# Kernel optimization log

Measured on AMD Instinct MI355X. Metric: run time of the kernel, lower is better.

## Reference

```python
import jax, jax.numpy as jnp
import numpy as np

N_NODES = 20000
N_EDGES = 320000
N_GRAPHS = 32
IN_CH = 5
HID = 64
HEADS = 4
DH = HID // HEADS  # 16
LAYERS = 8
EPS = 1e-5
SLOPE = 0.2


def setup_inputs() -> dict:
    key = jax.random.key(0)
    ks = jax.random.split(key, 32)
    inp = {}
    inp['x1'] = jax.random.normal(ks[0], (N_NODES, IN_CH), dtype=jnp.float32)
    inp['x2'] = jax.random.normal(ks[1], (N_NODES, IN_CH), dtype=jnp.float32)
    inp['edge_index1'] = jax.random.randint(ks[2], (2, N_EDGES), 0, N_NODES, dtype=jnp.int32)
    inp['edge_index2'] = jax.random.randint(ks[3], (2, N_EDGES), 0, N_NODES, dtype=jnp.int32)
    inp['batch1'] = jnp.sort(jax.random.randint(ks[4], (N_NODES,), 0, N_GRAPHS, dtype=jnp.int32))
    inp['batch2'] = jnp.sort(jax.random.randint(ks[5], (N_NODES,), 0, N_GRAPHS, dtype=jnp.int32))
    # node_lin
    inp['Wn'] = jax.random.normal(ks[6], (IN_CH, HID), dtype=jnp.float32) / np.sqrt(IN_CH)
    inp['bnode'] = jnp.zeros((HID,), dtype=jnp.float32)
    # GATv2 layers (stacked over LAYERS)
    s = 1.0 / np.sqrt(HID)
    inp['Wl'] = jax.random.normal(ks[7], (LAYERS, HID, HID), dtype=jnp.float32) * s
    inp['bl'] = jnp.zeros((LAYERS, HID), dtype=jnp.float32)
    inp['Wr'] = jax.random.normal(ks[8], (LAYERS, HID, HID), dtype=jnp.float32) * s
    inp['br'] = jnp.zeros((LAYERS, HID), dtype=jnp.float32)
    inp['att'] = jax.random.normal(ks[9], (LAYERS, HEADS, DH), dtype=jnp.float32) / np.sqrt(DH)
    inp['cbias'] = jnp.zeros((LAYERS, HID), dtype=jnp.float32)
    # batch norms
    inp['gamma'] = jnp.ones((LAYERS, HID), dtype=jnp.float32)
    inp['beta'] = jnp.zeros((LAYERS, HID), dtype=jnp.float32)
    # fc head
    inp['f1w'] = jax.random.normal(ks[10], (2 * HID, 256), dtype=jnp.float32) / np.sqrt(2 * HID)
    inp['f1b'] = jnp.zeros((256,), dtype=jnp.float32)
    inp['f2w'] = jax.random.normal(ks[11], (256, 128), dtype=jnp.float32) / np.sqrt(256)
    inp['f2b'] = jnp.zeros((128,), dtype=jnp.float32)
    inp['f3w'] = jax.random.normal(ks[12], (128, 1), dtype=jnp.float32) / np.sqrt(128)
    inp['f3b'] = jnp.zeros((1,), dtype=jnp.float32)
    return inp


def _gatv2_layer(x, src, dst, Wl, bl, Wr, br, att, bias):
    # x: [N, HID]; src/dst: [E'] (self loops included)
    N = x.shape[0]
    xl = (x @ Wl + bl).reshape(N, HEADS, DH)  # source transform
    xr = (x @ Wr + br).reshape(N, HEADS, DH)  # target transform
    e = jax.nn.leaky_relu(xl[src] + xr[dst], SLOPE)          # [E, H, DH]
    score = jnp.einsum('ehd,hd->eh', e, att)                  # [E, H]
    smax = jax.ops.segment_max(score, dst, num_segments=N)    # [N, H]
    ex = jnp.exp(score - smax[dst])
    denom = jax.ops.segment_sum(ex, dst, num_segments=N)
    alpha = ex / denom[dst]                                   # [E, H]
    msg = alpha[:, :, None] * xl[src]                         # [E, H, DH]
    out = jax.ops.segment_sum(msg, dst, num_segments=N)       # [N, H, DH]
    return out.reshape(N, HID) + bias


def _forward_once(x, edge_index, batch, Wn, bnode, Wl, bl, Wr, br, att, cbias, gamma, beta):
    N = x.shape[0]
    loop = jnp.arange(N, dtype=edge_index.dtype)
    src = jnp.concatenate([edge_index[0], loop])  # add_self_loops=True
    dst = jnp.concatenate([edge_index[1], loop])
    h = x @ Wn + bnode
    for l in range(LAYERS):
        g = _gatv2_layer(h, src, dst, Wl[l], bl[l], Wr[l], br[l], att[l], cbias[l])
        mu = g.mean(axis=0)
        var = g.var(axis=0)
        g = (g - mu) / jnp.sqrt(var + EPS) * gamma[l] + beta[l]
        h = h + jax.nn.elu(g)
    # global_mean_pool
    sums = jax.ops.segment_sum(h, batch, num_segments=N_GRAPHS)
    cnt = jax.ops.segment_sum(jnp.ones((N,), dtype=h.dtype), batch, num_segments=N_GRAPHS)
    return sums / jnp.maximum(cnt, 1.0)[:, None]


def reference(x1, edge_index1, batch1, x2, edge_index2, batch2, Wn, bnode, Wl, bl, Wr, br, att, cbias, gamma, beta, f1w, f1b, f2w, f2b, f3w, f3b):
    o1 = _forward_once(x1, edge_index1, batch1, Wn, bnode, Wl, bl, Wr, br, att, cbias, gamma, beta)
    o2 = _forward_once(x2, edge_index2, batch2, Wn, bnode, Wl, bl, Wr, br, att, cbias, gamma, beta)
    c = jnp.concatenate([o1, o2], axis=1)           # [G, 128]
    h = jax.nn.relu(c @ f1w + f1b)                   # dropout = identity (eval)
    h = jax.nn.relu(h @ f2w + f2b)
    return h @ f3w + f3b                             # [G, 1]
```

## Files before the change

kernel.cpp:

```cpp
#include <hip/hip_runtime.h>
#include <hip/hip_bf16.h>
#include <hip/hip_fp16.h>
#include <stdint.h>

#define N_NODES 20000
#define HID 64
#define EPS 1e-5f

typedef _Float16 h2 __attribute__((ext_vector_type(2)));

__device__ __forceinline__ h2 u2h(uint32_t u) { union { uint32_t u; h2 h; } v; v.u = u; return v.h; }

struct GP {
    const int* ei;
    const int* batch;
    const float* x;
    int* deg;
    int* cursor;
    int* csr;
    float* h;
    __half* xlh;
    __half* xrh;
    float* gb;
    float* stats;
    float* osum;
};


__global__ void k_csr_init(GP a, GP b, int n, int two) {
    int t = blockIdx.x * blockDim.x + threadIdx.x;
    if (t < n) {
        a.deg[t] = 1;
        if (two) b.deg[t] = 1;
    }
}

__global__ void k_count(GP a, GP b, int Ea, int Eb, int two) {
    int t = blockIdx.x * blockDim.x + threadIdx.x;
    if (t < Ea) atomicAdd(&a.deg[a.ei[Ea + t]], 1);
    if (two && t < Eb) atomicAdd(&b.deg[b.ei[Eb + t]], 1);
}

#define SCAN_T 1024
#define SCAN_C 20
__global__ __launch_bounds__(1024) void k_scan(GP a, GP b, int n, int totA, int totB) {
    GP g = blockIdx.x ? b : a;
    int total = blockIdx.x ? totB : totA;
    __shared__ int sd[SCAN_T];
    int t = threadIdx.x;
    int base = t * SCAN_C;
    int loc[SCAN_C];
    int s = 0;
#pragma unroll
    for (int i = 0; i < SCAN_C; ++i) {
        int idx = base + i;
        loc[i] = (idx < n) ? g.deg[idx] : 0;
        s += loc[i];
    }
    sd[t] = s;
    __syncthreads();
    for (int off = 1; off < SCAN_T; off <<= 1) {
        int v = (t >= off) ? sd[t - off] : 0;
        __syncthreads();
        sd[t] += v;
        __syncthreads();
    }
    int run = sd[t] - s;
#pragma unroll
    for (int i = 0; i < SCAN_C; ++i) {
        int idx = base + i;
        if (idx < n) { g.deg[idx] = run; g.cursor[idx] = run; run += loc[i]; }
    }
    if (t == 0) g.deg[n] = total;
}

__global__ void k_scatter(GP a, GP b, int Ea, int Eb, int n, int two) {
    int t = blockIdx.x * blockDim.x + threadIdx.x;
    if (t < Ea) {
        int s = a.ei[t], d = a.ei[Ea + t];
        a.csr[atomicAdd(&a.cursor[d], 1)] = s * 128;
    } else if (t < Ea + n) {
        int nn = t - Ea;
        a.csr[atomicAdd(&a.cursor[nn], 1)] = nn * 128;
    }
    if (two) {
        if (t < Eb) {
            int s = b.ei[t], d = b.ei[Eb + t];
            b.csr[atomicAdd(&b.cursor[d], 1)] = s * 128;
        } else if (t < Eb + n) {
            int nn = t - Eb;
            b.csr[atomicAdd(&b.cursor[nn], 1)] = nn * 128;
        }
    }
}


__global__ void k_wcvt(const float* __restrict__ Wl, const float* __restrict__ Wr,
                       uint32_t* __restrict__ wpk) {
    int t = blockIdx.x * 256 + threadIdx.x;
    if (t >= 16384) return;
    int l = t >> 11, r = t & 2047;
    int k2 = r >> 6, c = r & 63;
    const float* wl = Wl + l * 4096;
    const float* wr = Wr + l * 4096;
    h2 a, b;
    a.x = (_Float16)wl[(2 * k2) * 64 + c];
    a.y = (_Float16)wl[(2 * k2 + 1) * 64 + c];
    b.x = (_Float16)wr[(2 * k2) * 64 + c];
    b.y = (_Float16)wr[(2 * k2 + 1) * 64 + c];
    union { h2 h; uint32_t u; } ua, ub;
    ua.h = a; ub.h = b;
    wpk[l * 4096 + r] = ua.u;
    wpk[l * 4096 + 2048 + r] = ub.u;
}


__global__ void k_nodelin(GP a, GP b, int nPer, const float* __restrict__ Wn,
                          const float* __restrict__ bn, int n) {
    int bid = blockIdx.x;
    GP g = a;
    if (bid >= nPer) { g = b; bid -= nPer; }
    int idx = bid * 256 + threadIdx.x;
    if (idx >= n * HID) return;
    int node = idx >> 6, c = idx & 63;
    float acc = bn[c];
#pragma unroll
    for (int k = 0; k < 5; ++k) acc += g.x[node * 5 + k] * Wn[k * HID + c];
    g.h[idx] = acc;
}


__global__ __launch_bounds__(256) void k_lin2(GP ga, GP gbp, int nPer, int n,
        const uint32_t* __restrict__ wl2g, const float* __restrict__ bl,
        const uint32_t* __restrict__ wr2g, const float* __restrict__ br,
        const float* __restrict__ gamma, const float* __restrict__ beta, int layer) {
    __shared__ uint32_t wl2[2048], wr2[2048];
    __shared__ _Float16 hs16[2048];
    int bid = blockIdx.x;
    GP g = ga;
    if (bid >= nPer) { g = gbp; bid -= nPer; }
    {
        uint4* dl = (uint4*)wl2; const uint4* sl = (const uint4*)wl2g;
        uint4* dr = (uint4*)wr2; const uint4* sr = (const uint4*)wr2g;
        for (int i = threadIdx.x; i < 512; i += 256) { dl[i] = sl[i]; dr[i] = sr[i]; }
    }
    int c = threadIdx.x & 63;
    int wid = threadIdx.x >> 6;
    float blv = bl[c], brv = br[c];
    float mu = 0.f, inv = 1.f, gam = 1.f, bet = 0.f;
    if (layer > 0) {
        const float* st = g.stats + (layer - 1) * 128;
        float invn = 1.0f / (float)n;
        mu = st[c] * invn;
        float var = st[64 + c] * invn - mu * mu;
        inv = rsqrtf(fmaxf(var, 0.f) + EPS);
        gam = gamma[c]; bet = beta[c];
    }
    int nb = bid * 32 + wid * 8;
    size_t off0 = (size_t)nb * 64 + c;
    float hv[8];
    if (layer > 0) {
#pragma unroll
        for (int j = 0; j < 8; ++j) {
            float gv = g.gb[off0 + j * 64];
            float ov = g.h[off0 + j * 64];
            float v = (gv - mu) * inv * gam + bet;
            v = v > 0.f ? v : expm1f(v);
            hv[j] = ov + v;
            g.h[off0 + j * 64] = hv[j];
        }
    } else {
#pragma unroll
        for (int j = 0; j < 8; ++j) hv[j] = g.h[off0 + j * 64];
    }
    _Float16* hw16 = &hs16[wid * 512];
#pragma unroll
    for (int j = 0; j < 8; ++j) hw16[j * 64 + c] = (_Float16)hv[j];
    __syncthreads();
    const uint32_t* hw2 = (const uint32_t*)hw16;
    float accl[8], accr[8];
#pragma unroll
    for (int j = 0; j < 8; ++j) { accl[j] = blv; accr[j] = brv; }
    for (int k8 = 0; k8 < 8; ++k8) {
        uint4 hq[8];
#pragma unroll
        for (int j = 0; j < 8; ++j) hq[j] = *(const uint4*)&hw2[j * 32 + k8 * 4];
#pragma unroll
        for (int p = 0; p < 4; ++p) {
            h2 wlv = u2h(wl2[(k8 * 4 + p) * 64 + c]);
            h2 wrv = u2h(wr2[(k8 * 4 + p) * 64 + c]);
#pragma unroll
            for (int j = 0; j < 8; ++j) {
                h2 hp = u2h((&hq[j].x)[p]);
                accl[j] = __builtin_amdgcn_fdot2(hp, wlv, accl[j], false);
                accr[j] = __builtin_amdgcn_fdot2(hp, wrv, accr[j], false);
            }
        }
    }
#pragma unroll
    for (int j = 0; j < 8; ++j) {
        g.xlh[off0 + j * 64] = __float2half(accl[j]);
        g.xrh[off0 + j * 64] = __float2half(accr[j]);
    }
}


__device__ __forceinline__ float red8(float p) {
    p += __int_as_float(__builtin_amdgcn_update_dpp(0, __float_as_int(p), 0xB1, 0xF, 0xF, true));
    p += __int_as_float(__builtin_amdgcn_update_dpp(0, __float_as_int(p), 0x4E, 0xF, 0xF, true));
    p += __int_as_float(__builtin_amdgcn_update_dpp(0, __float_as_int(p), 0x141, 0xF, 0xF, true));
    return p;
}

__global__ __launch_bounds__(1024) void k_attn(GP ga, GP gbp, int nPer,
        const float* __restrict__ att, const float* __restrict__ cbias, int layer, int n) {
    int bid = blockIdx.x;
    GP g = (bid & 1) ? gbp : ga;
    bid >>= 1;
    int lane = threadIdx.x & 63;
    int wid = threadIdx.x >> 6;
    int hh = lane >> 5;
    int cl = lane & 31;
    int gw = bid * 16 + wid;
    int nw = nPer * 16;
    const float LOG2E = 1.44269504f;
    float a0 = att[2 * cl] * LOG2E;
    float a1 = att[2 * cl + 1] * LOG2E;
    float cb0 = cbias[2 * cl], cb1 = cbias[2 * cl + 1];
    const h2 slope = {(_Float16)0.2f, (_Float16)0.2f};
    const int* __restrict__ rowptr = g.deg;
    const int* __restrict__ csr = g.csr;
    const char* xlb = (const char*)g.xlh + (size_t)cl * 4;
    const char* xrb = (const char*)g.xrh + (size_t)cl * 4;
    float* __restrict__ gbuf = g.gb;
    float* st = g.stats + layer * 128;
    float bs0 = 0.f, bs1 = 0.f, bq0 = 0.f, bq1 = 0.f;
    for (int node = gw; node < n; node += nw) {
        int start = rowptr[node], end = rowptr[node + 1];
        h2 xrv = *(const h2*)(xrb + (size_t)node * 128);
        float sself;
        {
            h2 xs = *(const h2*)(xlb + (size_t)node * 128);
            h2 t = xs + xrv;
            h2 lk = __builtin_elementwise_max(t, t * slope);
            float sp = fmaf((float)lk.x, a0, (float)lk.y * a1);
            sself = red8(sp);
        }
        float lsum = 0.f, acc0 = 0.f, acc1 = 0.f;
        int idx = start;
        for (; idx + 16 <= end; idx += 16) {
            int off[8];
            h2 xv[8];
#pragma unroll
            for (int j = 0; j < 8; ++j) off[j] = csr[idx + 2 * j + hh];
#pragma unroll
            for (int j = 0; j < 8; ++j) xv[j] = *(const h2*)(xlb + off[j]);
#pragma unroll
            for (int j = 0; j < 8; ++j) {
                h2 t = xv[j] + xrv;
                h2 lk = __builtin_elementwise_max(t, t * slope);
                float sp = fmaf((float)lk.x, a0, (float)lk.y * a1);
                float w = exp2f(fminf(red8(sp) - sself, 110.f));
                lsum += w;
                acc0 = fmaf(w, (float)xv[j].x, acc0);
                acc1 = fmaf(w, (float)xv[j].y, acc1);
            }
        }
        for (; idx + 8 <= end; idx += 8) {
            int off[4];
            h2 xv[4];
#pragma unroll
            for (int j = 0; j < 4; ++j) off[j] = csr[idx + 2 * j + hh];
#pragma unroll
            for (int j = 0; j < 4; ++j) xv[j] = *(const h2*)(xlb + off[j]);
#pragma unroll
            for (int j = 0; j < 4; ++j) {
                h2 t = xv[j] + xrv;
                h2 lk = __builtin_elementwise_max(t, t * slope);
                float sp = fmaf((float)lk.x, a0, (float)lk.y * a1);
                float w = exp2f(fminf(red8(sp) - sself, 110.f));
                lsum += w;
                acc0 = fmaf(w, (float)xv[j].x, acc0);
                acc1 = fmaf(w, (float)xv[j].y, acc1);
            }
        }
        for (; idx < end; idx += 2) {
            int e = idx + hh;
            bool valid = e < end;
            int off = csr[valid ? e : end - 1];
            h2 xv = *(const h2*)(xlb + off);
            h2 t = xv + xrv;
            h2 lk = __builtin_elementwise_max(t, t * slope);
            float sp = fmaf((float)lk.x, a0, (float)lk.y * a1);
            float w = exp2f(fminf(red8(sp) - sself, 110.f));
            w = valid ? w : 0.f;
            lsum += w;
            acc0 = fmaf(w, (float)xv.x, acc0);
            acc1 = fmaf(w, (float)xv.y, acc1);
        }
        lsum += __shfl_xor(lsum, 32);
        acc0 += __shfl_xor(acc0, 32);
        acc1 += __shfl_xor(acc1, 32);
        if (hh == 0) {
            float invl = 1.0f / lsum;
            float o0 = acc0 * invl + cb0;
            float o1 = acc1 * invl + cb1;
            float2 o = {o0, o1};
            *(float2*)(gbuf + (size_t)node * 64 + 2 * cl) = o;
            bs0 += o0; bs1 += o1;
            bq0 += o0 * o0; bq1 += o1 * o1;
        }
    }
    __shared__ float2 sred[1024];
    float2 z = {0.f, 0.f};
    float2 v1 = {bs0, bs1};
    sred[threadIdx.x] = (hh == 0) ? v1 : z;
    __syncthreads();
    if (threadIdx.x < 32) {
        float t0 = 0.f, t1 = 0.f;
#pragma unroll
        for (int w = 0; w < 16; ++w) { float2 s = sred[w * 64 + threadIdx.x]; t0 += s.x; t1 += s.y; }
        atomicAdd(&st[2 * threadIdx.x], t0);
        atomicAdd(&st[2 * threadIdx.x + 1], t1);
    }
    __syncthreads();
    float2 v2 = {bq0, bq1};
    sred[threadIdx.x] = (hh == 0) ? v2 : z;
    __syncthreads();
    if (threadIdx.x < 32) {
        float t0 = 0.f, t1 = 0.f;
#pragma unroll
        for (int w = 0; w < 16; ++w) { float2 s = sred[w * 64 + threadIdx.x]; t0 += s.x; t1 += s.y; }
        atomicAdd(&st[64 + 2 * threadIdx.x], t0);
        atomicAdd(&st[64 + 2 * threadIdx.x + 1], t1);
    }
}


__global__ __launch_bounds__(256) void k_pool(GP ga, GP gbp, int nPer,
        const float* __restrict__ gamma, const float* __restrict__ beta, int n) {
    int bid = blockIdx.x;
    GP g = ga;
    if (bid >= nPer) { g = gbp; bid -= nPer; }
    int lane = threadIdx.x & 63, w = threadIdx.x >> 6;
    const float* st = g.stats + 7 * 128;
    float invn = 1.f / (float)n;
    float mu = st[lane] * invn;
    float var = st[64 + lane] * invn - mu * mu;
    float inv = rsqrtf(fmaxf(var, 0.f) + EPS);
    float gam = gamma[lane], bet = beta[lane];
    int chunk = (n + nPer - 1) / nPer;
    int s = bid * chunk;
    int e = min(s + chunk, n);
    float acc = 0.f;
    int cur = -1;
    for (int node = s + w; node < e; node += 4) {
        int bg = g.batch[node];
        size_t off = (size_t)node * 64 + lane;
        float gv = g.gb[off];
        float hv = g.h[off];
        float v = (gv - mu) * inv * gam + bet;
        float hn = hv + (v > 0.f ? v : expm1f(v));
        if (bg != cur) {
            if (cur >= 0) atomicAdd(&g.osum[cur * 64 + lane], acc);
            acc = 0.f; cur = bg;
        }
        acc += hn;
    }
    if (cur >= 0) atomicAdd(&g.osum[cur * 64 + lane], acc);
}


__device__ __forceinline__ int lb(const int* __restrict__ b, int n, int v) {
    int lo = 0, hi = n;
    while (lo < hi) { int mid = (lo + hi) >> 1; if (b[mid] < v) lo = mid + 1; else hi = mid; }
    return lo;
}

__global__ __launch_bounds__(256) void k_fc(const float* __restrict__ o1, const float* __restrict__ o2,
                                            const int* __restrict__ b1, const int* __restrict__ b2,
                                            const float* __restrict__ f1w, const float* __restrict__ f1b,
                                            const float* __restrict__ f2w, const float* __restrict__ f2b,
                                            const float* __restrict__ f3w, const float* __restrict__ f3b,
                                            float* __restrict__ out, int n) {
    int gid = blockIdx.x, t = threadIdx.x;
    __shared__ float cin[128];
    __shared__ float h1[256];
    __shared__ float red[128];
    __shared__ int cnts[2];
    if (t == 0) cnts[0] = lb(b1, n, gid + 1) - lb(b1, n, gid);
    if (t == 1) cnts[1] = lb(b2, n, gid + 1) - lb(b2, n, gid);
    __syncthreads();
    if (t < 64) {
        float c1 = (float)(cnts[0] > 0 ? cnts[0] : 1);
        float c2 = (float)(cnts[1] > 0 ? cnts[1] : 1);
        cin[t] = o1[gid * 64 + t] / c1;
        cin[64 + t] = o2[gid * 64 + t] / c2;
    }
    __syncthreads();
    float a = f1b[t];
#pragma unroll 8
    for (int k = 0; k < 128; ++k) a += cin[k] * f1w[k * 256 + t];
    h1[t] = fmaxf(a, 0.f);
    __syncthreads();
    if (t < 128) {
        float a2 = f2b[t];
#pragma unroll 8
        for (int k = 0; k < 256; ++k) a2 += h1[k] * f2w[k * 128 + t];
        red[t] = fmaxf(a2, 0.f) * f3w[t];
    }
    __syncthreads();
    for (int off = 64; off > 0; off >>= 1) {
        if (t < off) red[t] += red[t + off];
        __syncthreads();
    }
    if (t == 0) out[gid] = red[0] + f3b[0];
}


extern "C" void kernel_launch(void* const* d_in, const int* in_sizes, int n_in,
                              void* d_out, int out_size, void* d_ws, size_t ws_size,
                              hipStream_t stream) {
    const float* x1 = (const float*)d_in[0];
    const float* x2 = (const float*)d_in[1];
    const int* ei1 = (const int*)d_in[2];
    const int* ei2 = (const int*)d_in[3];
    const int* b1 = (const int*)d_in[4];
    const int* b2 = (const int*)d_in[5];
    const float* Wn = (const float*)d_in[6];
    const float* bnode = (const float*)d_in[7];
    const float* Wl = (const float*)d_in[8];
    const float* bl = (const float*)d_in[9];
    const float* Wr = (const float*)d_in[10];
    const float* br = (const float*)d_in[11];
    const float* att = (const float*)d_in[12];
    const float* cbias = (const float*)d_in[13];
    const float* gamma = (const float*)d_in[14];
    const float* beta = (const float*)d_in[15];
    const float* f1w = (const float*)d_in[16];
    const float* f1b = (const float*)d_in[17];
    const float* f2w = (const float*)d_in[18];
    const float* f2b = (const float*)d_in[19];
    const float* f3w = (const float*)d_in[20];
    const float* f3b = (const float*)d_in[21];
    float* out = (float*)d_out;

    const int N = N_NODES;
    const int EA = in_sizes[2] / 2;
    const int EB = in_sizes[3] / 2;
    const size_t INT_PG = 20096 + 20096 + 340096;
    const size_t BIG = (size_t)N * 64;
    const size_t SMALL = 2 * 1024 + 2 * 2048;
    const size_t WPK = 32768;
    const size_t dualBytes = 2 * INT_PG * 4 + (8 * BIG + SMALL + WPK) * 4;
    const int dual = (ws_size >= dualBytes) ? 1 : 0;

    int* ibase = (int*)d_ws;
    int* iA = ibase;
    int* iB = dual ? ibase + INT_PG : ibase;
    float* fbase = (float*)(ibase + (size_t)(dual ? 2 : 1) * INT_PG);
    float* hA = fbase;
    float* xlA = hA + BIG;
    float* xrA = xlA + BIG;
    float* gbA = xrA + BIG;
    float* hB = dual ? gbA + BIG : hA;
    float* xlB = dual ? hB + BIG : xlA;
    float* xrB = dual ? xlB + BIG : xrA;
    float* gbB = dual ? xrB + BIG : gbA;
    float* small = dual ? gbB + BIG : gbA + BIG;
    float* statsA = small;
    float* statsB = small + 1024;
    float* osumA = small + 2048;
    float* osumB = small + 4096;
    uint32_t* wpk = (uint32_t*)(small + SMALL);

    GP A, B;
    A.ei = ei1; A.batch = b1; A.x = x1;
    A.deg = iA; A.cursor = iA + 20096; A.csr = iA + 40192;
    A.h = hA; A.xlh = (__half*)xlA; A.xrh = (__half*)xrA;
    A.gb = gbA; A.stats = statsA; A.osum = osumA;
    B.ei = ei2; B.batch = b2; B.x = x2;
    B.deg = iB; B.cursor = iB + 20096; B.csr = iB + 40192;
    B.h = hB; B.xlh = (__half*)xlB; B.xrh = (__half*)xrB;
    B.gb = gbB; B.stats = statsB; B.osum = osumB;

    hipMemsetAsync(small, 0, SMALL * sizeof(float), stream);

    const int LIN2_NB = 625;
    const int ATT_NB = 256;
    const int POOL_NB = 250;

    if (dual) {
        int Emax = EA > EB ? EA : EB;
        k_csr_init<<<(N + 255) / 256, 256, 0, stream>>>(A, B, N, 1);
        k_count<<<(Emax + 255) / 256, 256, 0, stream>>>(A, B, EA, EB, 1);
        k_scan<<<2, 1024, 0, stream>>>(A, B, N, EA + N, EB + N);
        k_scatter<<<(Emax + N + 255) / 256, 256, 0, stream>>>(A, B, EA, EB, N, 1);
        k_wcvt<<<64, 256, 0, stream>>>(Wl, Wr, wpk);
        k_nodelin<<<2 * ((N * 64) / 256), 256, 0, stream>>>(A, B, (N * 64) / 256, Wn, bnode, N);
        for (int l = 0; l < 8; ++l) {
            const float* gm = l ? gamma + (l - 1) * 64 : gamma;
            const float* bt = l ? beta + (l - 1) * 64 : beta;
            k_lin2<<<2 * LIN2_NB, 256, 0, stream>>>(A, B, LIN2_NB, N,
                                                    wpk + l * 4096, bl + l * 64,
                                                    wpk + l * 4096 + 2048, br + l * 64, gm, bt, l);
            k_attn<<<2 * ATT_NB, 1024, 0, stream>>>(A, B, ATT_NB, att + l * 64, cbias + l * 64, l, N);
        }
        k_pool<<<2 * POOL_NB, 256, 0, stream>>>(A, B, POOL_NB, gamma + 7 * 64, beta + 7 * 64, N);
    } else {
        for (int gi = 0; gi < 2; ++gi) {
            GP G = gi ? B : A;
            int E = gi ? EB : EA;
            k_csr_init<<<(N + 255) / 256, 256, 0, stream>>>(G, G, N, 0);
            k_count<<<(E + 255) / 256, 256, 0, stream>>>(G, G, E, E, 0);
            k_scan<<<1, 1024, 0, stream>>>(G, G, N, E + N, E + N);
            k_scatter<<<(E + N + 255) / 256, 256, 0, stream>>>(G, G, E, E, N, 0);
            if (gi == 0) k_wcvt<<<64, 256, 0, stream>>>(Wl, Wr, wpk);
            k_nodelin<<<(N * 64) / 256, 256, 0, stream>>>(G, G, (N * 64) / 256, Wn, bnode, N);
            for (int l = 0; l < 8; ++l) {
                const float* gm = l ? gamma + (l - 1) * 64 : gamma;
                const float* bt = l ? beta + (l - 1) * 64 : beta;
                k_lin2<<<LIN2_NB, 256, 0, stream>>>(G, G, LIN2_NB, N,
                                                    wpk + l * 4096, bl + l * 64,
                                                    wpk + l * 4096 + 2048, br + l * 64, gm, bt, l);
                k_attn<<<2 * ATT_NB, 1024, 0, stream>>>(G, G, ATT_NB, att + l * 64, cbias + l * 64, l, N);
            }
            k_pool<<<POOL_NB, 256, 0, stream>>>(G, G, POOL_NB, gamma + 7 * 64, beta + 7 * 64, N);
        }
    }
    k_fc<<<32, 256, 0, stream>>>(osumA, osumB, b1, b2, f1w, f1b, f2w, f2b, f3w, f3b, out, N);
}
```

Before: 634.4 us.

## Fuse node_lin into first lin2, persistent tile loop, fdot2 attention scores

Removes the separate node-linear kernel by computing the input projection inside the layer-0 lin2 kernel. lin2 becomes grid-strided over 625 tiles with 320 blocks per graph, so each block loads the packed weights into shared memory once and reuses them across tiles. The attention score dot product switches to a packed half fdot2 with half-precision attention weights, trading some precision for fewer conversions. The tile loop has no barrier between the per-wave shared writes and reads, relying on each wave using only its own slice.

```diff
diff --git a/kernel.cpp b/kernel.cpp
--- a/kernel.cpp
+++ b/kernel.cpp
@@ -115,25 +115,11 @@
 }
 
 
-__global__ void k_nodelin(GP a, GP b, int nPer, const float* __restrict__ Wn,
-                          const float* __restrict__ bn, int n) {
-    int bid = blockIdx.x;
-    GP g = a;
-    if (bid >= nPer) { g = b; bid -= nPer; }
-    int idx = bid * 256 + threadIdx.x;
-    if (idx >= n * HID) return;
-    int node = idx >> 6, c = idx & 63;
-    float acc = bn[c];
-#pragma unroll
-    for (int k = 0; k < 5; ++k) acc += g.x[node * 5 + k] * Wn[k * HID + c];
-    g.h[idx] = acc;
-}
-
-
 __global__ __launch_bounds__(256) void k_lin2(GP ga, GP gbp, int nPer, int n,
         const uint32_t* __restrict__ wl2g, const float* __restrict__ bl,
         const uint32_t* __restrict__ wr2g, const float* __restrict__ br,
-        const float* __restrict__ gamma, const float* __restrict__ beta, int layer) {
+        const float* __restrict__ gamma, const float* __restrict__ beta,
+        const float* __restrict__ Wn, const float* __restrict__ bn, int layer) {
     __shared__ uint32_t wl2[2048], wr2[2048];
     __shared__ _Float16 hs16[2048];
     int bid = blockIdx.x;
@@ -148,6 +134,7 @@
     int wid = threadIdx.x >> 6;
     float blv = bl[c], brv = br[c];
     float mu = 0.f, inv = 1.f, gam = 1.f, bet = 0.f;
+    float wn_c[5], bnv = 0.f;
     if (layer > 0) {
         const float* st = g.stats + (layer - 1) * 128;
         float invn = 1.0f / (float)n;
@@ -155,52 +142,66 @@
         float var = st[64 + c] * invn - mu * mu;
         inv = rsqrtf(fmaxf(var, 0.f) + EPS);
         gam = gamma[c]; bet = beta[c];
-    }
-    int nb = bid * 32 + wid * 8;
-    size_t off0 = (size_t)nb * 64 + c;
-    float hv[8];
-    if (layer > 0) {
+    } else {
+#pragma unroll
+        for (int k = 0; k < 5; ++k) wn_c[k] = Wn[k * HID + c];
+        bnv = bn[c];
+    }
+    __syncthreads();
+    _Float16* hw16 = &hs16[wid * 512];
+    const uint32_t* hw2 = (const uint32_t*)hw16;
+    const int nTiles = 625;
+    for (int tile = bid; tile < nTiles; tile += nPer) {
+        int nb = tile * 32 + wid * 8;
+        size_t off0 = (size_t)nb * 64 + c;
+        float hv[8];
+        if (layer > 0) {
+#pragma unroll
+            for (int j = 0; j < 8; ++j) {
+                float gv = g.gb[off0 + j * 64];
+                float ov = g.h[off0 + j * 64];
+                float v = (gv - mu) * inv * gam + bet;
+                v = v > 0.f ? v : expm1f(v);
+                hv[j] = ov + v;
+                g.h[off0 + j * 64] = hv[j];
+            }
+        } else {
+#pragma unroll
+            for (int j = 0; j < 8; ++j) {
+                const float* xr = g.x + (size_t)(nb + j) * 5;
+                float acc = bnv;
+#pragma unroll
+                for (int k = 0; k < 5; ++k) acc = fmaf(xr[k], wn_c[k], acc);
+                hv[j] = acc;
+                g.h[off0 + j * 64] = acc;
+            }
+        }
+#pragma unroll
+        for (int j = 0; j < 8; ++j) hw16[j * 64 + c] = (_Float16)hv[j];
+        float accl[8], accr[8];
+#pragma unroll
+        for (int j = 0; j < 8; ++j) { accl[j] = blv; accr[j] = brv; }
+        for (int k8 = 0; k8 < 8; ++k8) {
+            uint4 hq[8];
+#pragma unroll
+            for (int j = 0; j < 8; ++j) hq[j] = *(const uint4*)&hw2[j * 32 + k8 * 4];
+#pragma unroll
+            for (int p = 0; p < 4; ++p) {
+                h2 wlv = u2h(wl2[(k8 * 4 + p) * 64 + c]);
+                h2 wrv = u2h(wr2[(k8 * 4 + p) * 64 + c]);
+#pragma unroll
+                for (int j = 0; j < 8; ++j) {
+                    h2 hp = u2h((&hq[j].x)[p]);
+                    accl[j] = __builtin_amdgcn_fdot2(hp, wlv, accl[j], false);
+                    accr[j] = __builtin_amdgcn_fdot2(hp, wrv, accr[j], false);
+                }
+            }
+        }
 #pragma unroll
         for (int j = 0; j < 8; ++j) {
-            float gv = g.gb[off0 + j * 64];
-            float ov = g.h[off0 + j * 64];
-            float v = (gv - mu) * inv * gam + bet;
-            v = v > 0.f ? v : expm1f(v);
-            hv[j] = ov + v;
-            g.h[off0 + j * 64] = hv[j];
-        }
-    } else {
-#pragma unroll
-        for (int j = 0; j < 8; ++j) hv[j] = g.h[off0 + j * 64];
-    }
-    _Float16* hw16 = &hs16[wid * 512];
-#pragma unroll
-    for (int j = 0; j < 8; ++j) hw16[j * 64 + c] = (_Float16)hv[j];
-    __syncthreads();
-    const uint32_t* hw2 = (const uint32_t*)hw16;
-    float accl[8], accr[8];
-#pragma unroll
-    for (int j = 0; j < 8; ++j) { accl[j] = blv; accr[j] = brv; }
-    for (int k8 = 0; k8 < 8; ++k8) {
-        uint4 hq[8];
-#pragma unroll
-        for (int j = 0; j < 8; ++j) hq[j] = *(const uint4*)&hw2[j * 32 + k8 * 4];
-#pragma unroll
-        for (int p = 0; p < 4; ++p) {
-            h2 wlv = u2h(wl2[(k8 * 4 + p) * 64 + c]);
-            h2 wrv = u2h(wr2[(k8 * 4 + p) * 64 + c]);
-#pragma unroll
-            for (int j = 0; j < 8; ++j) {
-                h2 hp = u2h((&hq[j].x)[p]);
-                accl[j] = __builtin_amdgcn_fdot2(hp, wlv, accl[j], false);
-                accr[j] = __builtin_amdgcn_fdot2(hp, wrv, accr[j], false);
-            }
-        }
-    }
-#pragma unroll
-    for (int j = 0; j < 8; ++j) {
-        g.xlh[off0 + j * 64] = __float2half(accl[j]);
-        g.xrh[off0 + j * 64] = __float2half(accr[j]);
+            g.xlh[off0 + j * 64] = __float2half(accl[j]);
+            g.xrh[off0 + j * 64] = __float2half(accr[j]);
+        }
     }
 }
 
@@ -224,8 +225,9 @@
     int gw = bid * 16 + wid;
     int nw = nPer * 16;
     const float LOG2E = 1.44269504f;
-    float a0 = att[2 * cl] * LOG2E;
-    float a1 = att[2 * cl + 1] * LOG2E;
+    h2 ap;
+    ap.x = (_Float16)(att[2 * cl] * LOG2E);
+    ap.y = (_Float16)(att[2 * cl + 1] * LOG2E);
     float cb0 = cbias[2 * cl], cb1 = cbias[2 * cl + 1];
     const h2 slope = {(_Float16)0.2f, (_Float16)0.2f};
     const int* __restrict__ rowptr = g.deg;
@@ -243,7 +245,7 @@
             h2 xs = *(const h2*)(xlb + (size_t)node * 128);
             h2 t = xs + xrv;
             h2 lk = __builtin_elementwise_max(t, t * slope);
-            float sp = fmaf((float)lk.x, a0, (float)lk.y * a1);
+            float sp = __builtin_amdgcn_fdot2(lk, ap, 0.f, false);
             sself = red8(sp);
         }
         float lsum = 0.f, acc0 = 0.f, acc1 = 0.f;
@@ -259,7 +261,7 @@
             for (int j = 0; j < 8; ++j) {
                 h2 t = xv[j] + xrv;
                 h2 lk = __builtin_elementwise_max(t, t * slope);
-                float sp = fmaf((float)lk.x, a0, (float)lk.y * a1);
+                float sp = __builtin_amdgcn_fdot2(lk, ap, 0.f, false);
                 float w = exp2f(fminf(red8(sp) - sself, 110.f));
                 lsum += w;
                 acc0 = fmaf(w, (float)xv[j].x, acc0);
@@ -277,7 +279,7 @@
             for (int j = 0; j < 4; ++j) {
                 h2 t = xv[j] + xrv;
                 h2 lk = __builtin_elementwise_max(t, t * slope);
-                float sp = fmaf((float)lk.x, a0, (float)lk.y * a1);
+                float sp = __builtin_amdgcn_fdot2(lk, ap, 0.f, false);
                 float w = exp2f(fminf(red8(sp) - sself, 110.f));
                 lsum += w;
                 acc0 = fmaf(w, (float)xv[j].x, acc0);
@@ -291,7 +293,7 @@
             h2 xv = *(const h2*)(xlb + off);
             h2 t = xv + xrv;
             h2 lk = __builtin_elementwise_max(t, t * slope);
-            float sp = fmaf((float)lk.x, a0, (float)lk.y * a1);
+            float sp = __builtin_amdgcn_fdot2(lk, ap, 0.f, false);
             float w = exp2f(fminf(red8(sp) - sself, 110.f));
             w = valid ? w : 0.f;
             lsum += w;
@@ -486,7 +488,7 @@
 
     hipMemsetAsync(small, 0, SMALL * sizeof(float), stream);
 
-    const int LIN2_NB = 625;
+    const int LIN2_NB = 320;
     const int ATT_NB = 256;
     const int POOL_NB = 250;
 
@@ -497,13 +499,13 @@
         k_scan<<<2, 1024, 0, stream>>>(A, B, N, EA + N, EB + N);
         k_scatter<<<(Emax + N + 255) / 256, 256, 0, stream>>>(A, B, EA, EB, N, 1);
         k_wcvt<<<64, 256, 0, stream>>>(Wl, Wr, wpk);
-        k_nodelin<<<2 * ((N * 64) / 256), 256, 0, stream>>>(A, B, (N * 64) / 256, Wn, bnode, N);
         for (int l = 0; l < 8; ++l) {
             const float* gm = l ? gamma + (l - 1) * 64 : gamma;
             const float* bt = l ? beta + (l - 1) * 64 : beta;
             k_lin2<<<2 * LIN2_NB, 256, 0, stream>>>(A, B, LIN2_NB, N,
                                                     wpk + l * 4096, bl + l * 64,
-                                                    wpk + l * 4096 + 2048, br + l * 64, gm, bt, l);
+                                                    wpk + l * 4096 + 2048, br + l * 64, gm, bt,
+                                                    Wn, bnode, l);
             k_attn<<<2 * ATT_NB, 1024, 0, stream>>>(A, B, ATT_NB, att + l * 64, cbias + l * 64, l, N);
         }
         k_pool<<<2 * POOL_NB, 256, 0, stream>>>(A, B, POOL_NB, gamma + 7 * 64, beta + 7 * 64, N);
@@ -516,13 +518,13 @@
             k_scan<<<1, 1024, 0, stream>>>(G, G, N, E + N, E + N);
             k_scatter<<<(E + N + 255) / 256, 256, 0, stream>>>(G, G, E, E, N, 0);
             if (gi == 0) k_wcvt<<<64, 256, 0, stream>>>(Wl, Wr, wpk);
-            k_nodelin<<<(N * 64) / 256, 256, 0, stream>>>(G, G, (N * 64) / 256, Wn, bnode, N);
             for (int l = 0; l < 8; ++l) {
                 const float* gm = l ? gamma + (l - 1) * 64 : gamma;
                 const float* bt = l ? beta + (l - 1) * 64 : beta;
                 k_lin2<<<LIN2_NB, 256, 0, stream>>>(G, G, LIN2_NB, N,
                                                     wpk + l * 4096, bl + l * 64,
-                                                    wpk + l * 4096 + 2048, br + l * 64, gm, bt, l);
+                                                    wpk + l * 4096 + 2048, br + l * 64, gm, bt,
+                                                    Wn, bnode, l);
                 k_attn<<<2 * ATT_NB, 1024, 0, stream>>>(G, G, ATT_NB, att + l * 64, cbias + l * 64, l, N);
             }
             k_pool<<<POOL_NB, 256, 0, stream>>>(G, G, POOL_NB, gamma + 7 * 64, beta + 7 * 64, N);
```

Result: slower. 690.1 us (+8.8%).
